# Optimization experiments

Hardware: AMD Instinct MI355X
Metric: run time of the kernel (lower is better)

The kernel has to match this reference:

```python
import jax, jax.numpy as jnp
import numpy as np

D, L, DIM, G = 64, 64, 512, 256      # dialogues, utterances/dialogue, feat dim, graph dim
TOPK_FRAC = 0.2
TAU = 0.07


def setup_inputs() -> dict:
    key = jax.random.key(0)
    ks = jax.random.split(key, 7)
    N = D * L
    t = jax.random.normal(ks[0], (N, DIM), dtype=jnp.float32)
    a = jax.random.normal(ks[1], (N, DIM), dtype=jnp.float32)
    v = jax.random.normal(ks[2], (N, DIM), dtype=jnp.float32)
    W_fc = jax.random.normal(ks[3], (DIM, G), dtype=jnp.float32) / np.sqrt(DIM)
    b_fc = jnp.zeros((G,), dtype=jnp.float32)
    W_h = jax.random.normal(ks[4], (G, G), dtype=jnp.float32) / np.sqrt(G)
    b_h = jnp.zeros((G,), dtype=jnp.float32)
    dia_len = np.full((D,), L, dtype=np.int64)  # uniform dialogue lengths
    return {"t": t, "a": a, "v": v, "W_fc": W_fc, "b_fc": b_fc,
            "W_h": W_h, "b_h": b_h, "dia_len": dia_len}


def _contrastive_loss(x, y, tau=TAU):
    # symmetric InfoNCE with matched-index positives
    xn = x / (jnp.linalg.norm(x, axis=-1, keepdims=True) + 1e-8)
    yn = y / (jnp.linalg.norm(y, axis=-1, keepdims=True) + 1e-8)
    sim = (xn @ yn.T) / tau                     # [N, N]
    pos_xy = jnp.diagonal(jax.nn.log_softmax(sim, axis=1))
    pos_yx = jnp.diagonal(jax.nn.log_softmax(sim, axis=0))
    return -(pos_xy.mean() + pos_yx.mean()) / 2.0


def _forward(t, a, v, W_fc, b_fc, W_h, b_h, dia_len):
    dl = np.asarray(dia_len)
    d, l = dl.shape[0], int(dl[0])              # uniform lengths assumed
    m = 3 * l                                   # nodes (and hyperedges) per dialogue
    k = int(l * TOPK_FRAC)
    dim = t.shape[-1]

    # per-dialogue node features in original order [t_i; a_i; v_i]
    feat = jnp.concatenate([t.reshape(d, l, dim),
                            a.reshape(d, l, dim),
                            v.reshape(d, l, dim)], axis=1)   # [d, m, dim]

    # squared euclidean distances (same ordering as torch.cdist for top-k smallest)
    sq = jnp.sum(feat * feat, axis=-1)                        # [d, m]
    d2 = sq[:, :, None] + sq[:, None, :] - 2.0 * jnp.einsum('dmf,dnf->dmn', feat, feat)
    d2 = jax.lax.stop_gradient(jnp.maximum(d2, 0.0))
    _, idx = jax.lax.top_k(-d2, k)                            # [d, m, k] nearest nodes

    # boolean incidence H[d, e, n] = node n participates in hyperedge e
    # (set-union dedup in the original == boolean OR here)
    node_ids = jnp.arange(m)
    H_nb = (idx[..., None] == node_ids).any(axis=2)           # [d, m, m]
    u = node_ids // 3                                         # central utterance of edge j
    cent = ((node_ids[None, :] == u[:, None]) |
            (node_ids[None, :] == u[:, None] + l) |
            (node_ids[None, :] == u[:, None] + 2 * l))        # [m, m]
    H = (H_nb | cent[None]).astype(feat.dtype)                # [d, m, m]

    # fc projection
    X = feat @ W_fc + b_fc                                    # [d, m, G]

    # hypergraph conv: node -> hyperedge (mean) -> node (mean), then Linear+ReLU
    deg_e = H.sum(axis=2, keepdims=True)                      # [d, m, 1]
    E = jnp.einsum('den,dng->deg', H, X) / deg_e              # edge features
    deg_v = H.sum(axis=1)[..., None]                          # [d, m, 1]
    Y = jnp.einsum('den,deg->dng', H, E) / deg_v              # node features
    out = jax.nn.relu(Y @ W_h + b_h)                          # [d, m, G]

    # reverse_features: regroup by modality across dialogues
    tn = out[:, :l].reshape(d * l, -1)
    an = out[:, l:2 * l].reshape(d * l, -1)
    vn = out[:, 2 * l:].reshape(d * l, -1)
    out_cat = jnp.concatenate([tn, an, vn], axis=1)           # [N, 3G]

    loss = (_contrastive_loss(tn, an) + _contrastive_loss(tn, vn)
            + _contrastive_loss(an, vn)) / 3.0
    return out_cat, loss


def reference(t, a, v, W_fc, b_fc, W_h, b_h, dia_len):
    return _forward(t, a, v, W_fc, b_fc, W_h, b_h, dia_len)
```

## Files before the change

### kernel.cpp

```cpp
#include <hip/hip_runtime.h>
#include <math.h>

#define NDIAL 64
#define M3    192
#define DIMF  512
#define GDIM  256
#define NROW  4096
#define TOPK  12
#define INV_TAU (1.0f/0.07f)

typedef __attribute__((ext_vector_type(8))) short bf16x8;
typedef __attribute__((ext_vector_type(4))) float f32x4;
typedef __attribute__((ext_vector_type(8))) ushort us8;
typedef _Float16 f16x8 __attribute__((ext_vector_type(8)));
typedef _Float16 f16x4v __attribute__((ext_vector_type(4)));
typedef __attribute__((address_space(3))) ushort lds_us;
typedef const __attribute__((address_space(1))) ushort gm_us;

__device__ __forceinline__ ushort f2bf(float f) {
    unsigned u = __float_as_uint(f);
    unsigned r = (u + 0x7fff + ((u >> 16) & 1)) >> 16;
    return (ushort)r;
}

template<int KD, int NW>
__device__ __forceinline__ void hgemm_bt(const _Float16* __restrict__ A, int lda,
                                         const _Float16* __restrict__ B, int ldb,
                                         f32x4 acc[4][4]) {
    __shared__ __align__(16) _Float16 As[64 * 40];
    __shared__ __align__(16) _Float16 Bs[NW * 64 * 40];
    const int tid = threadIdx.x;
    const int lane = tid & 63, w = tid >> 6;
    const int qd = lane >> 4, l15 = lane & 15;

#pragma unroll
    for (int fm = 0; fm < 4; fm++)
#pragma unroll
        for (int fn = 0; fn < 4; fn++)
            acc[fm][fn] = (f32x4){0.f, 0.f, 0.f, 0.f};

    for (int k0 = 0; k0 < KD; k0 += 32) {
        for (int f = tid; f < 256; f += NW * 64) {
            int row = f >> 2, c8 = f & 3;
            *(float4*)&As[row * 40 + c8 * 8] =
                *(const float4*)&A[(size_t)row * lda + k0 + c8 * 8];
        }
#pragma unroll
        for (int i = 0; i < 4; i++) {
            int f = tid + i * NW * 64;
            int row = f >> 2, c8 = f & 3;
            *(float4*)&Bs[row * 40 + c8 * 8] =
                *(const float4*)&B[(size_t)row * ldb + k0 + c8 * 8];
        }
        __syncthreads();
        f16x8 af[4], bfr[4];
#pragma unroll
        for (int fm = 0; fm < 4; fm++)
            af[fm] = *(const f16x8*)&As[(fm * 16 + l15) * 40 + qd * 8];
#pragma unroll
        for (int fn = 0; fn < 4; fn++)
            bfr[fn] = *(const f16x8*)&Bs[(w * 64 + fn * 16 + l15) * 40 + qd * 8];
#pragma unroll
        for (int fm = 0; fm < 4; fm++)
#pragma unroll
            for (int fn = 0; fn < 4; fn++)
                acc[fm][fn] = __builtin_amdgcn_mfma_f32_16x16x32_f16(
                    af[fm], bfr[fn], acc[fm][fn], 0, 0, 0);
        __syncthreads();
    }
}

__device__ __forceinline__ const float* node_ptr(const float* t, const float* a,
                                                 const float* v, int d, int j) {
    int mod = j >> 6, i = j & 63;
    const float* base = (mod == 0) ? t : (mod == 1) ? a : v;
    return base + (size_t)(d * 64 + i) * DIMF;
}

__global__ void kprep(const float* __restrict__ t, const float* __restrict__ a,
                      const float* __restrict__ v, const float* __restrict__ Wfc,
                      const float* __restrict__ Wh, _Float16* __restrict__ featb,
                      _Float16* __restrict__ featlo, _Float16* __restrict__ WfcT,
                      _Float16* __restrict__ WhT,
                      float* __restrict__ sq, float* __restrict__ rs,
                      float* __restrict__ cs, float* __restrict__ degV,
                      _Float16* __restrict__ HbT) {
    int b = blockIdx.x, tid = threadIdx.x;
    if (b < 6144) {
        int e = (b * 256 + tid) * 4;
        int d = e / (M3 * DIMF);
        int rem = e % (M3 * DIMF);
        int n = rem / DIMF, kk = rem % DIMF;
        int mod = n >> 6, i = n & 63;
        const float* src = ((mod == 0) ? t : (mod == 1) ? a : v)
                           + (size_t)(d * 64 + i) * DIMF + kk;
        float4 x = *(const float4*)src;
        _Float16 h0 = (_Float16)x.x, h1 = (_Float16)x.y;
        _Float16 h2 = (_Float16)x.z, h3 = (_Float16)x.w;
        f16x4v o = {h0, h1, h2, h3};
        *(f16x4v*)&featb[e] = o;
        f16x4v ol = {(_Float16)(x.x - (float)h0), (_Float16)(x.y - (float)h1),
                     (_Float16)(x.z - (float)h2), (_Float16)(x.w - (float)h3)};
        *(f16x4v*)&featlo[e] = ol;
    } else if (b < 6272) {
        int e = ((b - 6144) * 256 + tid) * 4;
        int g = e >> 9, kk = e & 511;
        f16x4v o = {(_Float16)Wfc[(size_t)(kk + 0) * GDIM + g],
                    (_Float16)Wfc[(size_t)(kk + 1) * GDIM + g],
                    (_Float16)Wfc[(size_t)(kk + 2) * GDIM + g],
                    (_Float16)Wfc[(size_t)(kk + 3) * GDIM + g]};
        *(f16x4v*)&WfcT[(size_t)g * DIMF + kk] = o;
    } else if (b < 6336) {
        int e = ((b - 6272) * 256 + tid) * 4;
        int go = e >> 8, g = e & 255;
        f16x4v o = {(_Float16)Wh[(size_t)(g + 0) * GDIM + go],
                    (_Float16)Wh[(size_t)(g + 1) * GDIM + go],
                    (_Float16)Wh[(size_t)(g + 2) * GDIM + go],
                    (_Float16)Wh[(size_t)(g + 3) * GDIM + go]};
        *(f16x4v*)&WhT[(size_t)go * GDIM + g] = o;
    } else if (b < 9408) {
        int lane = tid & 63, wv = tid >> 6;
        int n = (b - 6336) * 4 + wv;
        int d = n / M3, j = n % M3;
        const float4* s4 = (const float4*)node_ptr(t, a, v, d, j);
        float s = 0.f;
#pragma unroll
        for (int q = 0; q < 2; q++) {
            float4 x = s4[lane + q * 64];
            s += x.x * x.x + x.y * x.y + x.z * x.z + x.w * x.w;
        }
        for (int o = 32; o; o >>= 1) s += __shfl_down(s, o);
        if (lane == 0) sq[n] = s;
    } else if (b < 9456) {
        int i = (b - 9408) * 256 + tid;
        rs[i] = 0.f; cs[i] = 0.f; degV[i] = 0.f;
    } else {
        int i = (b - 9456) * 256 + tid;
        ulonglong2 z = {0ull, 0ull};
        *(ulonglong2*)&HbT[(size_t)i * 8] = z;
    }
}

__global__ __launch_bounds__(256) void k1_d2(const _Float16* __restrict__ featb,
                      const _Float16* __restrict__ featlo,
                      const float* __restrict__ sq,
                      float* __restrict__ d2) {
    int tileid = blockIdx.x;
    int d = blockIdx.y;
    int bi = (tileid < 3) ? 0 : (tileid < 5) ? 1 : 2;
    int bj = (tileid < 3) ? tileid : (tileid < 5) ? tileid - 2 : 2;
    const size_t base = (size_t)d * M3 * DIMF;
    const _Float16* Ah = featb  + base + (size_t)bi * 64 * DIMF;
    const _Float16* Al = featlo + base + (size_t)bi * 64 * DIMF;
    const _Float16* Bh = featb  + base + (size_t)bj * 64 * DIMF;
    const _Float16* Bl = featlo + base + (size_t)bj * 64 * DIMF;

    __shared__ __align__(16) _Float16 Ahs[64 * 40], Als[64 * 40];
    __shared__ __align__(16) _Float16 Bhs[64 * 40], Bls[64 * 40];
    const int tid = threadIdx.x;
    const int lane = tid & 63, w = tid >> 6;
    const int qd = lane >> 4, l15 = lane & 15;

    f32x4 acc[4];
#pragma unroll
    for (int fm = 0; fm < 4; fm++) acc[fm] = (f32x4){0.f, 0.f, 0.f, 0.f};

    for (int k0 = 0; k0 < DIMF; k0 += 32) {
        int row = tid >> 2, c8 = tid & 3;
        *(float4*)&Ahs[row * 40 + c8 * 8] = *(const float4*)&Ah[(size_t)row * DIMF + k0 + c8 * 8];
        *(float4*)&Als[row * 40 + c8 * 8] = *(const float4*)&Al[(size_t)row * DIMF + k0 + c8 * 8];
        *(float4*)&Bhs[row * 40 + c8 * 8] = *(const float4*)&Bh[(size_t)row * DIMF + k0 + c8 * 8];
        *(float4*)&Bls[row * 40 + c8 * 8] = *(const float4*)&Bl[(size_t)row * DIMF + k0 + c8 * 8];
        __syncthreads();
        f16x8 bh = *(const f16x8*)&Bhs[(w * 16 + l15) * 40 + qd * 8];
        f16x8 bl = *(const f16x8*)&Bls[(w * 16 + l15) * 40 + qd * 8];
#pragma unroll
        for (int fm = 0; fm < 4; fm++) {
            f16x8 ah = *(const f16x8*)&Ahs[(fm * 16 + l15) * 40 + qd * 8];
            f16x8 al = *(const f16x8*)&Als[(fm * 16 + l15) * 40 + qd * 8];
            acc[fm] = __builtin_amdgcn_mfma_f32_16x16x32_f16(ah, bh, acc[fm], 0, 0, 0);
            acc[fm] = __builtin_amdgcn_mfma_f32_16x16x32_f16(ah, bl, acc[fm], 0, 0, 0);
            acc[fm] = __builtin_amdgcn_mfma_f32_16x16x32_f16(al, bh, acc[fm], 0, 0, 0);
            acc[fm] = __builtin_amdgcn_mfma_f32_16x16x32_f16(al, bl, acc[fm], 0, 0, 0);
        }
        __syncthreads();
    }

    const float* sqd = sq + d * M3;
    float* outp = d2 + (size_t)d * M3 * M3;
#pragma unroll
    for (int fm = 0; fm < 4; fm++)
#pragma unroll
        for (int rg = 0; rg < 4; rg++) {
            int il = bi * 64 + fm * 16 + qd * 4 + rg;
            int jl = bj * 64 + w * 16 + l15;
            float vv = fmaxf(sqd[il] + sqd[jl] - 2.f * acc[fm][rg], 0.f);
            outp[(size_t)il * M3 + jl] = vv;
            if (bi != bj) outp[(size_t)jl * M3 + il] = vv;
        }
}

__global__ void k2_topk(const float* __restrict__ d2, _Float16* __restrict__ Hb,
                        _Float16* __restrict__ HbT, float* __restrict__ degE,
                        float* __restrict__ degV) {
    int lane = threadIdx.x & 63, wv = threadIdx.x >> 6;
    int r = blockIdx.x * 4 + wv;
    int d = r / M3, e = r % M3;
    const float* row = d2 + (size_t)r * M3;
    float w0 = row[lane], w1 = row[lane + 64], w2 = row[lane + 128];
    bool s0 = false, s1 = false, s2 = false;
#pragma unroll
    for (int it = 0; it < TOPK; it++) {
        float bv = w0; int bi = lane;
        if (w1 < bv) { bv = w1; bi = lane + 64; }
        if (w2 < bv) { bv = w2; bi = lane + 128; }
#pragma unroll
        for (int o = 1; o < 64; o <<= 1) {
            float ov = __shfl_xor(bv, o);
            int   oi = __shfl_xor(bi, o);
            if (ov < bv || (ov == bv && oi < bi)) { bv = ov; bi = oi; }
        }
        if (bi == lane)            { s0 = true; w0 = 3.4e38f; }
        else if (bi == lane + 64)  { s1 = true; w1 = 3.4e38f; }
        else if (bi == lane + 128) { s2 = true; w2 = 3.4e38f; }
    }
    int u = e / 3;
    if (lane == u) { s0 = true; s1 = true; s2 = true; }
    float f0 = s0 ? 1.f : 0.f, f1 = s1 ? 1.f : 0.f, f2 = s2 ? 1.f : 0.f;
    _Float16* Hrow = Hb + (size_t)r * M3;
    Hrow[lane] = (_Float16)f0;
    Hrow[lane + 64] = (_Float16)f1;
    Hrow[lane + 128] = (_Float16)f2;
    float cnt = f0 + f1 + f2;
#pragma unroll
    for (int o = 1; o < 64; o <<= 1) cnt += __shfl_xor(cnt, o);
    if (lane == 0) degE[r] = cnt;
    float* dv = degV + d * M3;
    _Float16* HT = HbT + (size_t)d * M3 * M3;
    if (s0) { atomicAdd(&dv[lane], 1.f);       HT[(size_t)lane * M3 + e] = (_Float16)1.f; }
    if (s1) { atomicAdd(&dv[lane + 64], 1.f);  HT[(size_t)(lane + 64) * M3 + e] = (_Float16)1.f; }
    if (s2) { atomicAdd(&dv[lane + 128], 1.f); HT[(size_t)(lane + 128) * M3 + e] = (_Float16)1.f; }
}

__global__ void k3_x(const _Float16* __restrict__ WfcT, const _Float16* __restrict__ featb,
                     const float* __restrict__ bfc, _Float16* __restrict__ XT) {
    int gb = blockIdx.x, d = blockIdx.y;
    const _Float16* A = WfcT + (size_t)gb * 64 * DIMF;
    const _Float16* B = featb + (size_t)d * M3 * DIMF;
    f32x4 acc[4][4];
    hgemm_bt<DIMF, 3>(A, DIMF, B, DIMF, acc);
    int lane = threadIdx.x & 63, w = threadIdx.x >> 6;
    int qd = lane >> 4, l15 = lane & 15;
    _Float16* out = XT + (size_t)d * GDIM * M3;
#pragma unroll
    for (int fm = 0; fm < 4; fm++)
#pragma unroll
        for (int rg = 0; rg < 4; rg++) {
            int g = gb * 64 + fm * 16 + qd * 4 + rg;
            float bias = bfc[g];
#pragma unroll
            for (int fn = 0; fn < 4; fn++) {
                int n = w * 64 + fn * 16 + l15;
                out[(size_t)g * M3 + n] = (_Float16)(acc[fm][fn][rg] + bias);
            }
        }
}

__global__ void k4_E(const _Float16* __restrict__ XT, const _Float16* __restrict__ Hb,
                     const float* __restrict__ degE, _Float16* __restrict__ ET) {
    int gb = blockIdx.x, d = blockIdx.y;
    const _Float16* A = XT + (size_t)d * GDIM * M3 + (size_t)gb * 64 * M3;
    const _Float16* B = Hb + (size_t)d * M3 * M3;
    f32x4 acc[4][4];
    hgemm_bt<M3, 3>(A, M3, B, M3, acc);
    int lane = threadIdx.x & 63, w = threadIdx.x >> 6;
    int qd = lane >> 4, l15 = lane & 15;
    float ide[4];
#pragma unroll
    for (int fn = 0; fn < 4; fn++)
        ide[fn] = 1.f / degE[d * M3 + w * 64 + fn * 16 + l15];
    _Float16* out = ET + (size_t)d * GDIM * M3;
#pragma unroll
    for (int fm = 0; fm < 4; fm++)
#pragma unroll
        for (int rg = 0; rg < 4; rg++) {
            int g = gb * 64 + fm * 16 + qd * 4 + rg;
#pragma unroll
            for (int fn = 0; fn < 4; fn++) {
                int e = w * 64 + fn * 16 + l15;
                out[(size_t)g * M3 + e] = (_Float16)(acc[fm][fn][rg] * ide[fn]);
            }
        }
}

__global__ void k5_Y(const _Float16* __restrict__ HbT, const _Float16* __restrict__ ET,
                     const float* __restrict__ degV, _Float16* __restrict__ Y) {
    int nb = blockIdx.x, d = blockIdx.y;
    const _Float16* A = HbT + (size_t)d * M3 * M3 + (size_t)nb * 64 * M3;
    const _Float16* B = ET + (size_t)d * GDIM * M3;
    f32x4 acc[4][4];
    hgemm_bt<M3, 4>(A, M3, B, M3, acc);
    int lane = threadIdx.x & 63, w = threadIdx.x >> 6;
    int qd = lane >> 4, l15 = lane & 15;
    _Float16* out = Y + ((size_t)d * M3 + nb * 64) * GDIM;
#pragma unroll
    for (int fm = 0; fm < 4; fm++)
#pragma unroll
        for (int rg = 0; rg < 4; rg++) {
            int ml = fm * 16 + qd * 4 + rg;
            float idv = 1.f / degV[d * M3 + nb * 64 + ml];
#pragma unroll
            for (int fn = 0; fn < 4; fn++) {
                int g = w * 64 + fn * 16 + l15;
                out[(size_t)ml * GDIM + g] = (_Float16)(acc[fm][fn][rg] * idv);
            }
        }
}

__global__ __launch_bounds__(256) void k6_out(const _Float16* __restrict__ Y,
                                              const _Float16* __restrict__ WhT,
                                              const float* __restrict__ bh,
                                              float* __restrict__ outp,
                                              ushort* __restrict__ xnb) {
    __shared__ float tile[64 * 256];
    __shared__ float ssq[64];
    int b = blockIdx.x, tid = threadIdx.x;
    if (tid < 64) ssq[tid] = 0.f;
    const _Float16* A = Y + (size_t)b * 64 * GDIM;
    f32x4 acc[4][4];
    hgemm_bt<GDIM, 4>(A, GDIM, WhT, GDIM, acc);
    int lane = tid & 63, w = tid >> 6;
    int qd = lane >> 4, l15 = lane & 15;
    int d = b / 3, mod = b % 3;
    float bb[4];
#pragma unroll
    for (int fn = 0; fn < 4; fn++)
        bb[fn] = bh[w * 64 + fn * 16 + l15];
#pragma unroll
    for (int fm = 0; fm < 4; fm++)
#pragma unroll
        for (int rg = 0; rg < 4; rg++) {
            int i = fm * 16 + qd * 4 + rg;
            float* orow = outp + (size_t)(d * 64 + i) * 768 + mod * GDIM;
            float s2 = 0.f;
#pragma unroll
            for (int fn = 0; fn < 4; fn++) {
                int go = w * 64 + fn * 16 + l15;
                float vv = fmaxf(acc[fm][fn][rg] + bb[fn], 0.f);
                orow[go] = vv;
                tile[i * 256 + go] = vv;
                s2 += vv * vv;
            }
            s2 += __shfl_xor(s2, 1);
            s2 += __shfl_xor(s2, 2);
            s2 += __shfl_xor(s2, 4);
            s2 += __shfl_xor(s2, 8);
            if (l15 == 0) atomicAdd(&ssq[i], s2);
        }
    __syncthreads();
    if (tid < 64) ssq[tid] = 1.f / (sqrtf(ssq[tid]) + 1e-8f);
    __syncthreads();
#pragma unroll
    for (int it = 0; it < 8; it++) {
        int f = tid + it * 256;
        int row = f >> 5, c = f & 31;
        float4 xa = *(const float4*)&tile[row * 256 + c * 8];
        float4 xb = *(const float4*)&tile[row * 256 + c * 8 + 4];
        float iv = ssq[row];
        us8 o = {f2bf(xa.x * iv), f2bf(xa.y * iv), f2bf(xa.z * iv), f2bf(xa.w * iv),
                 f2bf(xb.x * iv), f2bf(xb.y * iv), f2bf(xb.z * iv), f2bf(xb.w * iv)};
        int rx = d * 64 + row;
        int slot = (c & 24) | ((c & 7) ^ (row & 7));
        *(us8*)&xnb[((size_t)mod * NROW + rx) * GDIM + slot * 8] = o;
    }
}

#define TILE9 128
#define STAGE9(ELT)                                                        \
    {                                                                      \
        __builtin_amdgcn_global_load_lds(pa0 + (ELT), la0, 16, 0, 0);      \
        __builtin_amdgcn_global_load_lds(pb0 + (ELT), lb0, 16, 0, 0);      \
        __builtin_amdgcn_global_load_lds(pa1 + (ELT), la1, 16, 0, 0);      \
        __builtin_amdgcn_global_load_lds(pb1 + (ELT), lb1, 16, 0, 0);      \
        __builtin_amdgcn_global_load_lds(pa2 + (ELT), la2, 16, 0, 0);      \
        __builtin_amdgcn_global_load_lds(pb2 + (ELT), lb2, 16, 0, 0);      \
        __builtin_amdgcn_global_load_lds(pa3 + (ELT), la3, 16, 0, 0);      \
        __builtin_amdgcn_global_load_lds(pb3 + (ELT), lb3, 16, 0, 0);      \
    }
__global__ __launch_bounds__(256, 4) void k9_mfma(const ushort* __restrict__ xnb,
                                                  float* __restrict__ rs,
                                                  float* __restrict__ cs,
                                                  float* __restrict__ diag) {
    int lin = blockIdx.x + (blockIdx.y << 5) + (blockIdx.z << 10);
    int vid = (lin >> 3) + (lin & 7) * 384;
    int p  = vid >> 10;
    int r0 = vid & 1023;
    int ci = r0 >> 5, cj = r0 & 31;
    int px = (p == 2) ? 1 : 0;
    int py = (p == 0) ? 1 : 2;
    const ushort* A = xnb + ((size_t)px * NROW + ci * TILE9) * GDIM;
    const ushort* B = xnb + ((size_t)py * NROW + cj * TILE9) * GDIM;

    __shared__ __align__(16) ushort As[TILE9 * 64];
    __shared__ __align__(16) ushort Bs[TILE9 * 64];

    const int tid = threadIdx.x;
    const int lane = tid & 63, w = tid >> 6;
    const int wrow = w >> 1, wcol = w & 1;
    const int qd = lane >> 4, l15 = lane & 15;
    const int lrow = lane >> 3, lslot = lane & 7;

    const int rbase = w * 32 + lrow;
    const int cbase = lslot * 8;
    const gm_us* pa0 = (gm_us*)(A + (size_t)(rbase +  0) * GDIM + cbase);
    const gm_us* pa1 = (gm_us*)(A + (size_t)(rbase +  8) * GDIM + cbase);
    const gm_us* pa2 = (gm_us*)(A + (size_t)(rbase + 16) * GDIM + cbase);
    const gm_us* pa3 = (gm_us*)(A + (size_t)(rbase + 24) * GDIM + cbase);
    const gm_us* pb0 = (gm_us*)(B + (size_t)(rbase +  0) * GDIM + cbase);
    const gm_us* pb1 = (gm_us*)(B + (size_t)(rbase +  8) * GDIM + cbase);
    const gm_us* pb2 = (gm_us*)(B + (size_t)(rbase + 16) * GDIM + cbase);
    const gm_us* pb3 = (gm_us*)(B + (size_t)(rbase + 24) * GDIM + cbase);
    lds_us* la0 = (lds_us*)&As[(w * 32 +  0) * 64];
    lds_us* la1 = (lds_us*)&As[(w * 32 +  8) * 64];
    lds_us* la2 = (lds_us*)&As[(w * 32 + 16) * 64];
    lds_us* la3 = (lds_us*)&As[(w * 32 + 24) * 64];
    lds_us* lb0 = (lds_us*)&Bs[(w * 32 +  0) * 64];
    lds_us* lb1 = (lds_us*)&Bs[(w * 32 +  8) * 64];
    lds_us* lb2 = (lds_us*)&Bs[(w * 32 + 16) * 64];
    lds_us* lb3 = (lds_us*)&Bs[(w * 32 + 24) * 64];

    f32x4 acc[4][4] = {};

    auto compute = [&]() {
#pragma unroll
        for (int kk = 0; kk < 2; kk++) {
            bf16x8 af[4], bfv[4];
#pragma unroll
            for (int fm = 0; fm < 4; fm++) {
                int ar = wrow * 64 + fm * 16 + l15;
                af[fm] = *(const bf16x8*)&As[ar * 64 + ((kk * 4 + qd) ^ (ar & 7)) * 8];
            }
#pragma unroll
            for (int fn = 0; fn < 4; fn++) {
                int br = wcol * 64 + fn * 16 + l15;
                bfv[fn] = *(const bf16x8*)&Bs[br * 64 + ((kk * 4 + qd) ^ (br & 7)) * 8];
            }
#pragma unroll
            for (int fm = 0; fm < 4; fm++)
#pragma unroll
                for (int fn = 0; fn < 4; fn++)
                    acc[fm][fn] = __builtin_amdgcn_mfma_f32_16x16x32_bf16(
                        af[fm], bfv[fn], acc[fm][fn], 0, 0, 0);
        }
    };

    STAGE9(0);   __syncthreads(); compute(); __syncthreads();
    STAGE9(64);  __syncthreads(); compute(); __syncthreads();
    STAGE9(128); __syncthreads(); compute(); __syncthreads();
    STAGE9(192); __syncthreads(); compute(); __syncthreads();

    const float C2 = INV_TAU * 1.44269504088896f;
    f32x4 rv[4] = {};
    f32x4 cv[4] = {};
#pragma unroll
    for (int fm = 0; fm < 4; fm++)
#pragma unroll
        for (int fn = 0; fn < 4; fn++) {
            f32x4 sv = acc[fm][fn] * C2;
            f32x4 ev;
#pragma unroll
            for (int rg = 0; rg < 4; rg++)
                ev[rg] = exp2f(sv[rg]);
            rv[fm] += ev;
            cv[fn] += ev;
        }
    if (ci == cj) {
#pragma unroll
        for (int fm = 0; fm < 4; fm++)
#pragma unroll
            for (int fn = 0; fn < 4; fn++)
#pragma unroll
                for (int rg = 0; rg < 4; rg++) {
                    int lr = wrow * 64 + fm * 16 + qd * 4 + rg;
                    int lc = wcol * 64 + fn * 16 + l15;
                    if (lr == lc)
                        diag[p * NROW + ci * TILE9 + lr] = acc[fm][fn][rg] * INV_TAU;
                }
    }
#pragma unroll
    for (int fm = 0; fm < 4; fm++)
#pragma unroll
        for (int rg = 0; rg < 4; rg++) {
            float s = rv[fm][rg];
            s += __shfl_xor(s, 1);
            s += __shfl_xor(s, 2);
            s += __shfl_xor(s, 4);
            s += __shfl_xor(s, 8);
            if (l15 == 0)
                atomicAdd(&rs[p * NROW + ci * TILE9 + wrow * 64 + fm * 16 + qd * 4 + rg], s);
        }
#pragma unroll
    for (int fn = 0; fn < 4; fn++) {
        float s = (cv[fn][0] + cv[fn][1]) + (cv[fn][2] + cv[fn][3]);
        s += __shfl_xor(s, 16);
        s += __shfl_xor(s, 32);
        if (qd == 0)
            atomicAdd(&cs[p * NROW + cj * TILE9 + wcol * 64 + fn * 16 + l15], s);
    }
}

__global__ void k10_loss(const float* __restrict__ diag, const float* __restrict__ rs,
                         const float* __restrict__ cs, float* __restrict__ outp) {
    float acc = 0.f;
    for (int i = threadIdx.x; i < 3 * NROW; i += 256)
        acc += 2.f * diag[i] - logf(rs[i]) - logf(cs[i]);
    int lane = threadIdx.x & 63, wv = threadIdx.x >> 6;
    for (int o = 32; o; o >>= 1) acc += __shfl_down(acc, o);
    __shared__ float red[4];
    if (lane == 0) red[wv] = acc;
    __syncthreads();
    if (threadIdx.x == 0) {
        float tot = red[0] + red[1] + red[2] + red[3];
        outp[(size_t)NROW * 768] = -tot / (NROW * 6.0f);
    }
}

extern "C" void kernel_launch(void* const* d_in, const int* in_sizes, int n_in,
                              void* d_out, int out_size, void* d_ws, size_t ws_size,
                              hipStream_t stream) {
    const float* t   = (const float*)d_in[0];
    const float* a   = (const float*)d_in[1];
    const float* v   = (const float*)d_in[2];
    const float* Wfc = (const float*)d_in[3];
    const float* bfc = (const float*)d_in[4];
    const float* Wh  = (const float*)d_in[5];
    const float* bh  = (const float*)d_in[6];
    float* outp = (float*)d_out;
    float* ws = (float*)d_ws;

    float* sq    = ws;
    float* d2    = sq + 12288;
    float* HbF   = d2 + 2359296;
    float* HbTF  = HbF + 1179648;
    float* degE  = HbTF + 1179648;
    float* degV  = degE + 12288;
    float* featF = degV + 12288;
    float* WfcTF = featF + 3145728;
    float* WhTF  = WfcTF + 65536;
    float* XTF   = WhTF + 32768;
    float* ETF   = XTF + 1572864;
    float* YF    = ETF + 1572864;
    float* rs    = YF + 1572864;
    float* cs    = rs + 12288;
    float* diag  = cs + 12288;

    _Float16* Hb    = (_Float16*)HbF;
    _Float16* HbT   = (_Float16*)HbTF;
    _Float16* featb = (_Float16*)featF;
    _Float16* WfcT  = (_Float16*)WfcTF;
    _Float16* WhT   = (_Float16*)WhTF;
    _Float16* XT    = (_Float16*)XTF;
    _Float16* ET    = (_Float16*)ETF;
    _Float16* Y     = (_Float16*)YF;
    ushort*   xnb   = (ushort*)d2;
    _Float16* featlo = (_Float16*)XTF;

    kprep  <<<10608, 256, 0, stream>>>(t, a, v, Wfc, Wh, featb, featlo, WfcT,
                                       WhT, sq, rs, cs, degV, HbT);
    k1_d2  <<<dim3(6, 64), 256, 0, stream>>>(featb, featlo, sq, d2);
    k2_topk<<<3072, 256, 0, stream>>>(d2, Hb, HbT, degE, degV);
    k3_x   <<<dim3(4, 64), 192, 0, stream>>>(WfcT, featb, bfc, XT);
    k4_E   <<<dim3(4, 64), 192, 0, stream>>>(XT, Hb, degE, ET);
    k5_Y   <<<dim3(3, 64), 256, 0, stream>>>(HbT, ET, degV, Y);
    k6_out <<<192, 256, 0, stream>>>(Y, WhT, bh, outp, xnb);
    k9_mfma<<<dim3(32, 32, 3), 256, 0, stream>>>(xnb, rs, cs, diag);
    k10_loss<<<1, 256, 0, stream>>>(diag, rs, cs, outp);
}
```

Before: 263.7 us.

## Fuse X/E and Y/output GEMM pairs keeping intermediates in LDS

Merges the feature projection with the node-to-hyperedge aggregation, and the hyperedge-to-node aggregation with the output linear layer, into two kernels. The intermediate X and Y tiles stay in shared memory instead of being written to and re-read from global memory. This removes two kernel launches and the associated global traffic. The cost is larger LDS usage per block, which can reduce occupancy.

```diff
diff --git a/kernel.cpp b/kernel.cpp
--- a/kernel.cpp
+++ b/kernel.cpp
@@ -21,53 +21,6 @@
     unsigned u = __float_as_uint(f);
     unsigned r = (u + 0x7fff + ((u >> 16) & 1)) >> 16;
     return (ushort)r;
-}
-
-template<int KD, int NW>
-__device__ __forceinline__ void hgemm_bt(const _Float16* __restrict__ A, int lda,
-                                         const _Float16* __restrict__ B, int ldb,
-                                         f32x4 acc[4][4]) {
-    __shared__ __align__(16) _Float16 As[64 * 40];
-    __shared__ __align__(16) _Float16 Bs[NW * 64 * 40];
-    const int tid = threadIdx.x;
-    const int lane = tid & 63, w = tid >> 6;
-    const int qd = lane >> 4, l15 = lane & 15;
-
-#pragma unroll
-    for (int fm = 0; fm < 4; fm++)
-#pragma unroll
-        for (int fn = 0; fn < 4; fn++)
-            acc[fm][fn] = (f32x4){0.f, 0.f, 0.f, 0.f};
-
-    for (int k0 = 0; k0 < KD; k0 += 32) {
-        for (int f = tid; f < 256; f += NW * 64) {
-            int row = f >> 2, c8 = f & 3;
-            *(float4*)&As[row * 40 + c8 * 8] =
-                *(const float4*)&A[(size_t)row * lda + k0 + c8 * 8];
-        }
-#pragma unroll
-        for (int i = 0; i < 4; i++) {
-            int f = tid + i * NW * 64;
-            int row = f >> 2, c8 = f & 3;
-            *(float4*)&Bs[row * 40 + c8 * 8] =
-                *(const float4*)&B[(size_t)row * ldb + k0 + c8 * 8];
-        }
-        __syncthreads();
-        f16x8 af[4], bfr[4];
-#pragma unroll
-        for (int fm = 0; fm < 4; fm++)
-            af[fm] = *(const f16x8*)&As[(fm * 16 + l15) * 40 + qd * 8];
-#pragma unroll
-        for (int fn = 0; fn < 4; fn++)
-            bfr[fn] = *(const f16x8*)&Bs[(w * 64 + fn * 16 + l15) * 40 + qd * 8];
-#pragma unroll
-        for (int fm = 0; fm < 4; fm++)
-#pragma unroll
-            for (int fn = 0; fn < 4; fn++)
-                acc[fm][fn] = __builtin_amdgcn_mfma_f32_16x16x32_f16(
-                    af[fm], bfr[fn], acc[fm][fn], 0, 0, 0);
-        __syncthreads();
-    }
 }
 
 __device__ __forceinline__ const float* node_ptr(const float* t, const float* a,
@@ -242,39 +195,101 @@
     if (s2) { atomicAdd(&dv[lane + 128], 1.f); HT[(size_t)(lane + 128) * M3 + e] = (_Float16)1.f; }
 }
 
-__global__ void k3_x(const _Float16* __restrict__ WfcT, const _Float16* __restrict__ featb,
-                     const float* __restrict__ bfc, _Float16* __restrict__ XT) {
+__global__ __launch_bounds__(192) void k34_XE(const _Float16* __restrict__ WfcT,
+                      const _Float16* __restrict__ featb,
+                      const float* __restrict__ bfc,
+                      const _Float16* __restrict__ Hb,
+                      const float* __restrict__ degE,
+                      _Float16* __restrict__ ET) {
     int gb = blockIdx.x, d = blockIdx.y;
     const _Float16* A = WfcT + (size_t)gb * 64 * DIMF;
     const _Float16* B = featb + (size_t)d * M3 * DIMF;
+    const _Float16* H = Hb + (size_t)d * M3 * M3;
+
+    __shared__ __align__(16) _Float16 As[64 * 40];
+    __shared__ __align__(16) _Float16 Bs[M3 * 40];
+    __shared__ __align__(16) _Float16 Xls[64 * 200];
+    const int tid = threadIdx.x;
+    const int lane = tid & 63, w = tid >> 6;
+    const int qd = lane >> 4, l15 = lane & 15;
+
     f32x4 acc[4][4];
-    hgemm_bt<DIMF, 3>(A, DIMF, B, DIMF, acc);
-    int lane = threadIdx.x & 63, w = threadIdx.x >> 6;
-    int qd = lane >> 4, l15 = lane & 15;
-    _Float16* out = XT + (size_t)d * GDIM * M3;
+#pragma unroll
+    for (int fm = 0; fm < 4; fm++)
+#pragma unroll
+        for (int fn = 0; fn < 4; fn++) acc[fm][fn] = (f32x4){0.f, 0.f, 0.f, 0.f};
+
+    for (int k0 = 0; k0 < DIMF; k0 += 32) {
+        for (int f = tid; f < 256; f += 192) {
+            int row = f >> 2, c8 = f & 3;
+            *(float4*)&As[row * 40 + c8 * 8] =
+                *(const float4*)&A[(size_t)row * DIMF + k0 + c8 * 8];
+        }
+#pragma unroll
+        for (int i = 0; i < 4; i++) {
+            int f = tid + i * 192;
+            int row = f >> 2, c8 = f & 3;
+            *(float4*)&Bs[row * 40 + c8 * 8] =
+                *(const float4*)&B[(size_t)row * DIMF + k0 + c8 * 8];
+        }
+        __syncthreads();
+        f16x8 af[4], bfr[4];
+#pragma unroll
+        for (int fm = 0; fm < 4; fm++)
+            af[fm] = *(const f16x8*)&As[(fm * 16 + l15) * 40 + qd * 8];
+#pragma unroll
+        for (int fn = 0; fn < 4; fn++)
+            bfr[fn] = *(const f16x8*)&Bs[(w * 64 + fn * 16 + l15) * 40 + qd * 8];
+#pragma unroll
+        for (int fm = 0; fm < 4; fm++)
+#pragma unroll
+            for (int fn = 0; fn < 4; fn++)
+                acc[fm][fn] = __builtin_amdgcn_mfma_f32_16x16x32_f16(
+                    af[fm], bfr[fn], acc[fm][fn], 0, 0, 0);
+        __syncthreads();
+    }
 #pragma unroll
     for (int fm = 0; fm < 4; fm++)
 #pragma unroll
         for (int rg = 0; rg < 4; rg++) {
-            int g = gb * 64 + fm * 16 + qd * 4 + rg;
-            float bias = bfc[g];
+            int row = fm * 16 + qd * 4 + rg;
+            float bias = bfc[gb * 64 + row];
 #pragma unroll
             for (int fn = 0; fn < 4; fn++) {
-                int n = w * 64 + fn * 16 + l15;
-                out[(size_t)g * M3 + n] = (_Float16)(acc[fm][fn][rg] + bias);
+                int col = w * 64 + fn * 16 + l15;
+                Xls[row * 200 + col] = (_Float16)(acc[fm][fn][rg] + bias);
             }
         }
-}
-
-__global__ void k4_E(const _Float16* __restrict__ XT, const _Float16* __restrict__ Hb,
-                     const float* __restrict__ degE, _Float16* __restrict__ ET) {
-    int gb = blockIdx.x, d = blockIdx.y;
-    const _Float16* A = XT + (size_t)d * GDIM * M3 + (size_t)gb * 64 * M3;
-    const _Float16* B = Hb + (size_t)d * M3 * M3;
-    f32x4 acc[4][4];
-    hgemm_bt<M3, 3>(A, M3, B, M3, acc);
-    int lane = threadIdx.x & 63, w = threadIdx.x >> 6;
-    int qd = lane >> 4, l15 = lane & 15;
+    __syncthreads();
+
+#pragma unroll
+    for (int fm = 0; fm < 4; fm++)
+#pragma unroll
+        for (int fn = 0; fn < 4; fn++) acc[fm][fn] = (f32x4){0.f, 0.f, 0.f, 0.f};
+    for (int k0 = 0; k0 < M3; k0 += 32) {
+#pragma unroll
+        for (int i = 0; i < 4; i++) {
+            int f = tid + i * 192;
+            int row = f >> 2, c8 = f & 3;
+            *(float4*)&Bs[row * 40 + c8 * 8] =
+                *(const float4*)&H[(size_t)row * M3 + k0 + c8 * 8];
+        }
+        __syncthreads();
+        f16x8 af[4], bfr[4];
+#pragma unroll
+        for (int fm = 0; fm < 4; fm++)
+            af[fm] = *(const f16x8*)&Xls[(fm * 16 + l15) * 200 + k0 + qd * 8];
+#pragma unroll
+        for (int fn = 0; fn < 4; fn++)
+            bfr[fn] = *(const f16x8*)&Bs[(w * 64 + fn * 16 + l15) * 40 + qd * 8];
+#pragma unroll
+        for (int fm = 0; fm < 4; fm++)
+#pragma unroll
+            for (int fn = 0; fn < 4; fn++)
+                acc[fm][fn] = __builtin_amdgcn_mfma_f32_16x16x32_f16(
+                    af[fm], bfr[fn], acc[fm][fn], 0, 0, 0);
+        __syncthreads();
+    }
     float ide[4];
 #pragma unroll
     for (int fn = 0; fn < 4; fn++)
@@ -293,16 +308,63 @@
         }
 }
 
-__global__ void k5_Y(const _Float16* __restrict__ HbT, const _Float16* __restrict__ ET,
-                     const float* __restrict__ degV, _Float16* __restrict__ Y) {
+__global__ __launch_bounds__(256) void k56_Yout(const _Float16* __restrict__ HbT,
+                      const _Float16* __restrict__ ET,
+                      const float* __restrict__ degV,
+                      const _Float16* __restrict__ WhT,
+                      const float* __restrict__ bh,
+                      float* __restrict__ outp,
+                      ushort* __restrict__ xnb) {
     int nb = blockIdx.x, d = blockIdx.y;
     const _Float16* A = HbT + (size_t)d * M3 * M3 + (size_t)nb * 64 * M3;
     const _Float16* B = ET + (size_t)d * GDIM * M3;
+
+    __shared__ __align__(16) _Float16 As[64 * 40];
+    __shared__ __align__(16) _Float16 Bs[GDIM * 40];
+    __shared__ __align__(16) _Float16 Yls[64 * 264];
+    __shared__ float tile[64 * 256];
+    __shared__ float ssq[64];
+    const int tid = threadIdx.x;
+    const int lane = tid & 63, w = tid >> 6;
+    const int qd = lane >> 4, l15 = lane & 15;
+    if (tid < 64) ssq[tid] = 0.f;
+
     f32x4 acc[4][4];
-    hgemm_bt<M3, 4>(A, M3, B, M3, acc);
-    int lane = threadIdx.x & 63, w = threadIdx.x >> 6;
-    int qd = lane >> 4, l15 = lane & 15;
-    _Float16* out = Y + ((size_t)d * M3 + nb * 64) * GDIM;
+#pragma unroll
+    for (int fm = 0; fm < 4; fm++)
+#pragma unroll
+        for (int fn = 0; fn < 4; fn++) acc[fm][fn] = (f32x4){0.f, 0.f, 0.f, 0.f};
+
+    for (int k0 = 0; k0 < M3; k0 += 32) {
+        {
+            int f = tid;
+            int row = f >> 2, c8 = f & 3;
+            *(float4*)&As[row * 40 + c8 * 8] =
+                *(const float4*)&A[(size_t)row * M3 + k0 + c8 * 8];
+        }
+#pragma unroll
+        for (int i = 0; i < 4; i++) {
+            int f = tid + i * 256;
+            int row = f >> 2, c8 = f & 3;
+            *(float4*)&Bs[row * 40 + c8 * 8] =
+                *(const float4*)&B[(size_t)row * M3 + k0 + c8 * 8];
+        }
+        __syncthreads();
+        f16x8 af[4], bfr[4];
+#pragma unroll
+        for (int fm = 0; fm < 4; fm++)
+            af[fm] = *(const f16x8*)&As[(fm * 16 + l15) * 40 + qd * 8];
+#pragma unroll
+        for (int fn = 0; fn < 4; fn++)
+            bfr[fn] = *(const f16x8*)&Bs[(w * 64 + fn * 16 + l15) * 40 + qd * 8];
+#pragma unroll
+        for (int fm = 0; fm < 4; fm++)
+#pragma unroll
+            for (int fn = 0; fn < 4; fn++)
+                acc[fm][fn] = __builtin_amdgcn_mfma_f32_16x16x32_f16(
+                    af[fm], bfr[fn], acc[fm][fn], 0, 0, 0);
+        __syncthreads();
+    }
 #pragma unroll
     for (int fm = 0; fm < 4; fm++)
 #pragma unroll
@@ -312,26 +374,41 @@
 #pragma unroll
             for (int fn = 0; fn < 4; fn++) {
                 int g = w * 64 + fn * 16 + l15;
-                out[(size_t)ml * GDIM + g] = (_Float16)(acc[fm][fn][rg] * idv);
+                Yls[ml * 264 + g] = (_Float16)(acc[fm][fn][rg] * idv);
             }
         }
-}
-
-__global__ __launch_bounds__(256) void k6_out(const _Float16* __restrict__ Y,
-                                              const _Float16* __restrict__ WhT,
-                                              const float* __restrict__ bh,
-                                              float* __restrict__ outp,
-                                              ushort* __restrict__ xnb) {
-    __shared__ float tile[64 * 256];
-    __shared__ float ssq[64];
-    int b = blockIdx.x, tid = threadIdx.x;
-    if (tid < 64) ssq[tid] = 0.f;
-    const _Float16* A = Y + (size_t)b * 64 * GDIM;
-    f32x4 acc[4][4];
-    hgemm_bt<GDIM, 4>(A, GDIM, WhT, GDIM, acc);
-    int lane = tid & 63, w = tid >> 6;
-    int qd = lane >> 4, l15 = lane & 15;
-    int d = b / 3, mod = b % 3;
+    __syncthreads();
+
+#pragma unroll
+    for (int fm = 0; fm < 4; fm++)
+#pragma unroll
+        for (int fn = 0; fn < 4; fn++) acc[fm][fn] = (f32x4){0.f, 0.f, 0.f, 0.f};
+    for (int k0 = 0; k0 < GDIM; k0 += 32) {
+#pragma unroll
+        for (int i = 0; i < 4; i++) {
+            int f = tid + i * 256;
+            int row = f >> 2, c8 = f & 3;
+            *(float4*)&Bs[row * 40 + c8 * 8] =
+                *(const float4*)&WhT[(size_t)row * GDIM + k0 + c8 * 8];
+        }
+        __syncthreads();
+        f16x8 af[4], bfr[4];
+#pragma unroll
+        for (int fm = 0; fm < 4; fm++)
+            af[fm] = *(const f16x8*)&Yls[(fm * 16 + l15) * 264 + k0 + qd * 8];
+#pragma unroll
+        for (int fn = 0; fn < 4; fn++)
+            bfr[fn] = *(const f16x8*)&Bs[(w * 64 + fn * 16 + l15) * 40 + qd * 8];
+#pragma unroll
+        for (int fm = 0; fm < 4; fm++)
+#pragma unroll
+            for (int fn = 0; fn < 4; fn++)
+                acc[fm][fn] = __builtin_amdgcn_mfma_f32_16x16x32_f16(
+                    af[fm], bfr[fn], acc[fm][fn], 0, 0, 0);
+        __syncthreads();
+    }
+
+    int mod = nb;
     float bb[4];
 #pragma unroll
     for (int fn = 0; fn < 4; fn++)
@@ -559,9 +636,7 @@
     _Float16* featb = (_Float16*)featF;
     _Float16* WfcT  = (_Float16*)WfcTF;
     _Float16* WhT   = (_Float16*)WhTF;
-    _Float16* XT    = (_Float16*)XTF;
     _Float16* ET    = (_Float16*)ETF;
-    _Float16* Y     = (_Float16*)YF;
     ushort*   xnb   = (ushort*)d2;
     _Float16* featlo = (_Float16*)XTF;
 
@@ -569,10 +644,8 @@
                                        WhT, sq, rs, cs, degV, HbT);
     k1_d2  <<<dim3(6, 64), 256, 0, stream>>>(featb, featlo, sq, d2);
     k2_topk<<<3072, 256, 0, stream>>>(d2, Hb, HbT, degE, degV);
-    k3_x   <<<dim3(4, 64), 192, 0, stream>>>(WfcT, featb, bfc, XT);
-    k4_E   <<<dim3(4, 64), 192, 0, stream>>>(XT, Hb, degE, ET);
-    k5_Y   <<<dim3(3, 64), 256, 0, stream>>>(HbT, ET, degV, Y);
-    k6_out <<<192, 256, 0, stream>>>(Y, WhT, bh, outp, xnb);
+    k34_XE <<<dim3(4, 64), 192, 0, stream>>>(WfcT, featb, bfc, Hb, degE, ET);
+    k56_Yout<<<dim3(3, 64), 256, 0, stream>>>(HbT, ET, degV, WhT, bh, outp, xnb);
     k9_mfma<<<dim3(32, 32, 3), 256, 0, stream>>>(xnb, rs, cs, diag);
     k10_loss<<<1, 256, 0, stream>>>(diag, rs, cs, outp);
 }
```

Result: no change. 259.6 us (-1.5%).
